# Performance work log

Hardware: AMD Instinct MI355X
Metric: run time of the kernel (lower is better)

Reference implementation:

```python
import jax, jax.numpy as jnp
import numpy as np

PLP_ORDER = 16
N_CHANNEL = 40
FFT_LENGTH = 512
SAMPLE_RATE = 16000
LIFTER = 22
COMP_FACTOR = 0.33
FLOOR = 1e-5
F_MIN = 0.0
F_MAX = SAMPLE_RATE / 2


def _hz_to_mel(hz):
    return 1127.0 * np.log1p(np.asarray(hz, dtype=np.float64) / 700.0)


def _mel_to_hz(mel):
    return 700.0 * np.expm1(np.asarray(mel, dtype=np.float64) / 1127.0)


def _build_constants():
    # SPTK-style mel filter bank (triangular in mel domain).
    mel_min = _hz_to_mel(F_MIN)
    mel_max = _hz_to_mel(F_MAX)
    lower_bin = max(1, int(F_MIN / SAMPLE_RATE * FFT_LENGTH + 1.5))
    upper_bin = min(FFT_LENGTH // 2, int(F_MAX / SAMPLE_RATE * FFT_LENGTH + 0.5))
    seed = np.arange(1, N_CHANNEL + 2)
    cf_mel = (mel_max - mel_min) / (N_CHANNEL + 1) * seed + mel_min  # (C+1,)
    bins = np.arange(lower_bin, upper_bin)
    mel = _hz_to_mel(SAMPLE_RATE * bins / FFT_LENGTH)
    ch = np.searchsorted(cf_mel, mel, side='left')  # first center freq >= mel
    diff = cf_mel - np.concatenate([[mel_min], cf_mel[:-1]])
    w = (cf_mel[ch] - mel) / diff[ch]
    H = np.zeros((len(bins), N_CHANNEL))
    rows = np.arange(len(bins))
    low = ch - 1
    m_lo = low >= 0
    H[rows[m_lo], low[m_lo]] += w[m_lo]
    m_hi = ch <= N_CHANNEL - 1
    H[rows[m_hi], ch[m_hi]] += 1.0 - w[m_hi]
    # Equal-loudness curve over the first C center frequencies (in Hz).
    cf_hz = _mel_to_hz(cf_mel)
    f2 = cf_hz[:N_CHANNEL] ** 2
    eql = (f2 / (f2 + 160000.0)) ** 2 * (f2 + 1440000.0) / (f2 + 9610000.0)
    # Liftering vector, v[0] = 2.
    m = np.arange(PLP_ORDER + 1)
    lift = 1.0 + LIFTER / 2.0 * np.sin(np.pi / LIFTER * m)
    lift[0] = 2.0
    return lower_bin, upper_bin, H.astype(np.float32), eql.astype(np.float32), lift.astype(np.float32)


LOWER_BIN, UPPER_BIN, H_NP, EQL_NP, LIFT_NP = _build_constants()


def _levinson_durbin(r):
    # r: (..., M+1) autocorrelation -> (gain K, LPC coefficients a_1..a_M)
    M = PLP_ORDER
    E = r[..., 0]
    a = jnp.zeros(r.shape[:-1] + (M,), r.dtype)
    for i in range(1, M + 1):
        acc = r[..., i]
        if i > 1:
            acc = acc + jnp.einsum('...j,...j->...', a[..., : i - 1], r[..., 1:i][..., ::-1])
        k = -acc / E
        if i > 1:
            a = a.at[..., : i - 1].set(a[..., : i - 1] + k[..., None] * a[..., : i - 1][..., ::-1])
        a = a.at[..., i - 1].set(k)
        E = E * (1.0 - k * k)
    return jnp.sqrt(E), a


def _lpc_to_cepstrum(K, a):
    # c0 = log K; c_m = -a_m - sum_{k=1}^{m-1} (k/m) c_k a_{m-k}
    M = PLP_ORDER
    c = [jnp.log(K)]
    for m in range(1, M + 1):
        acc = a[..., m - 1]
        for k in range(1, m):
            acc = acc + (k / m) * c[k] * a[..., m - k - 1]
        c.append(-acc)
    return jnp.stack(c, axis=-1)  # (..., M+1)


def _plp(x):
    H = jnp.asarray(H_NP)
    eql = jnp.asarray(EQL_NP)
    lift = jnp.asarray(LIFT_NP)
    # Mel filter bank on power spectrum (use_power=True)
    fb = jnp.matmul(x[..., LOWER_BIN:UPPER_BIN], H)          # (..., C)
    logfb = jnp.log(jnp.maximum(fb, FLOOR))
    # Equal-loudness scaling + cubic-root amplitude compression
    y = (jnp.exp(logfb) * eql) ** COMP_FACTOR                # (..., C)
    # replicate1: duplicate first and last channels
    y = jnp.concatenate([y[..., :1], y, y[..., -1:]], axis=-1)  # (..., C+2)
    n = y.shape[-1]
    # hfft with norm='forward' -> inverse-FFT-like autocorrelation
    r = jnp.fft.hfft(y) / (2 * (n - 1))
    r = r[..., : PLP_ORDER + 1]
    K, a = _levinson_durbin(r)
    c = _lpc_to_cepstrum(K, a)
    c = c * lift
    return c[..., 1:]  # out_format 'y': PLP without C0, (..., M)


def setup_inputs() -> dict:
    key = jax.random.key(0)
    x = jax.random.uniform(key, (32, 4096, FFT_LENGTH // 2 + 1), dtype=jnp.float32)
    return {"x": x}


def reference(x):
    return _plp(x)
```

## Files before the change

kernel.cpp:

```cpp
#include <hip/hip_runtime.h>

#define NCH    40
#define MORD   16
#define NR     17
#define NBINS  257

namespace cfg {

constexpr double PI  = 3.14159265358979323846264338327950288;
constexpr double LN2 = 0.693147180559945309417232121458176568;

constexpr double cexp(double x) {
    double t = 1.0, s = 1.0;
    for (int i = 1; i < 40; ++i) { t *= x / i; s += t; }
    return s;
}

constexpr double clog(double z) {
    double lg = 0.0;
    while (z > 1.4142135623730951) { z *= 0.5; lg += LN2; }
    while (z < 0.7071067811865476) { z *= 2.0; lg -= LN2; }
    double u = (z - 1.0) / (z + 1.0), u2 = u * u, t = u, s = u;
    for (int k = 1; k < 24; ++k) { t *= u2; s += t / (2.0 * k + 1.0); }
    return lg + 2.0 * s;
}

constexpr double ccos(double x) {
    double tp = 2.0 * PI;
    double q = x / tp;
    long long k = (long long)(q + (q >= 0.0 ? 0.5 : -0.5));
    double r = x - (double)k * tp;
    double r2 = r * r, t = 1.0, s = 1.0;
    for (int i = 1; i < 20; ++i) { t *= -r2 / ((2.0 * i - 1.0) * (2.0 * i)); s += t; }
    return s;
}

constexpr double csin(double x) { return ccos(x - PI / 2.0); }

struct Tab {
    int   start[43];
    int   chan[257];
    float w[257];
    float eql[NCH];
    float lift[NR];
    float ctf[NR][21];
    constexpr Tab() : start(), chan(), w(), eql(), lift(), ctf() {
        const double lmax  = clog(87.0 / 7.0);
        const double U1127 = lmax / 41.0;
        for (int c = 0; c <= 41; ++c) {
            double thr = 22.4 * (cexp((double)c * U1127) - 1.0);
            int s = (int)thr + 1;
            if (s < 1) s = 1;
            if (s > 256) s = 256;
            start[c] = s;
        }
        start[42] = start[41];
        for (int c = 0; c <= 40; ++c) {
            for (int b = start[c]; b < start[c + 1]; ++b) {
                double mel = 1127.0 * clog(1.0 + (double)b * 31.25 / 700.0);
                double t   = mel / (1127.0 * U1127);
                w[b] = (float)(t - (double)c);
                chan[b] = c;
            }
        }
        for (int c = 0; c < NCH; ++c) {
            double cf = 700.0 * (cexp((double)(c + 1) * U1127) - 1.0);
            double f2 = cf * cf;
            double e  = f2 / (f2 + 160000.0);
            e = e * e * (f2 + 1440000.0) / (f2 + 9610000.0);
            eql[c] = (float)e;
        }
        for (int m = 0; m < NR; ++m)
            lift[m] = (float)(1.0 + 11.0 * csin(PI * (double)m / 22.0));
        lift[0] = 2.0f;
        for (int l = 0; l < NR; ++l)
            for (int j = 0; j <= 20; ++j) {
                double s = (j == 0) ? 1.0 : 2.0;
                ctf[l][j] = (float)(s * ccos(PI * (double)(j * l) / 41.0) / 82.0);
            }
    }
};

constexpr Tab T{};

}

template<int S>
__device__ __forceinline__ void fbank_path(const float* __restrict__ x,
                                           long long fg, float fb[NCH])
{
    using cfg::T;
    const long long B = fg * 257 + 1 - S;
    const float4* p4 = reinterpret_cast<const float4*>(x + B);
    float4 a = p4[0];
    #pragma unroll
    for (int j = 0; j < 64; ++j) {
        float4 b;
        if (S > 0 || j < 63) b = p4[j + 1]; else b = a;
        float e0, e1, e2, e3;
        if      (S == 0) { e0 = a.x; e1 = a.y; e2 = a.z; e3 = a.w; }
        else if (S == 1) { e0 = a.y; e1 = a.z; e2 = a.w; e3 = b.x; }
        else if (S == 2) { e0 = a.z; e1 = a.w; e2 = b.x; e3 = b.y; }
        else             { e0 = a.w; e1 = b.x; e2 = b.y; e3 = b.z; }
        const float ee[4] = { e0, e1, e2, e3 };
        #pragma unroll
        for (int q = 0; q < 4; ++q) {
            const int   bb = 4 * j + 1 + q;
            const int   ch = T.chan[bb];
            const float wa = T.w[bb];
            if (ch < NCH) fb[ch]     = fmaf(wa, ee[q], fb[ch]);
            if (ch >= 1)  fb[ch - 1] = fmaf(1.0f - wa, ee[q], fb[ch - 1]);
        }
        a = b;
    }
}

__global__ __launch_bounds__(256, 2) void plp_kernel(const float* __restrict__ x,
                                                     float* __restrict__ out,
                                                     int nframes)
{
    using cfg::T;
    const int tid  = threadIdx.x;
    const int lane = tid & 63;
    const long long GW = (long long)blockIdx.x * 4 + (tid >> 6);
    const int       r  = (int)(GW & 3);
    const long long q  = GW >> 2;
    const long long fg = (long long)r + 4 * (q * 64 + lane);
    if (fg >= nframes) return;

    float fb[NCH];
    #pragma unroll
    for (int c = 0; c < NCH; ++c) fb[c] = 0.f;

    switch (r) {
        case 0:  fbank_path<1>(x, fg, fb); break;
        case 1:  fbank_path<2>(x, fg, fb); break;
        case 2:  fbank_path<3>(x, fg, fb); break;
        default: fbank_path<0>(x, fg, fb); break;
    }

    float yv[NCH];
    #pragma unroll
    for (int c = 0; c < NCH; ++c) {
        float v = fmaxf(fb[c], 1e-5f) * T.eql[c];
        yv[c] = __expf(0.33f * __logf(v));
    }

    float ye[21], yo[21];
    ye[0] = yv[0] + yv[39];  yo[0] = yv[0] - yv[39];
    #pragma unroll
    for (int jj = 1; jj <= 20; ++jj) {
        float aa = yv[jj - 1], bb = yv[40 - jj];
        ye[jj] = aa + bb;  yo[jj] = aa - bb;
    }

    float rr[NR];
    #pragma unroll
    for (int lg = 0; lg < NR; ++lg) {
        const float* yy = (lg & 1) ? yo : ye;
        float acc = 0.f;
        #pragma unroll
        for (int jj = 0; jj <= 20; ++jj) acc = fmaf(T.ctf[lg][jj], yy[jj], acc);
        rr[lg] = acc;
    }

    float a[MORD];
    #pragma unroll
    for (int i = 0; i < MORD; ++i) a[i] = 0.f;
    float E = rr[0];
    #pragma unroll
    for (int i = 1; i <= MORD; ++i) {
        float acc = rr[i];
        #pragma unroll
        for (int jj = 0; jj < i - 1; ++jj) acc = fmaf(a[jj], rr[i - 1 - jj], acc);
        float k = -acc * __builtin_amdgcn_rcpf(E);
        const int half = (i - 1) / 2;
        #pragma unroll
        for (int jj = 0; jj < half; ++jj) {
            float t1 = a[jj], t2 = a[i - 2 - jj];
            a[jj]         = fmaf(k, t2, t1);
            a[i - 2 - jj] = fmaf(k, t1, t2);
        }
        if ((i - 1) & 1) a[half] = fmaf(k, a[half], a[half]);
        a[i - 1] = k;
        E = E * (1.f - k * k);
    }

    float cc[NR], ccs[NR];
    #pragma unroll
    for (int m = 1; m <= MORD; ++m) {
        float acc = 0.f;
        #pragma unroll
        for (int k2 = 1; k2 < m; ++k2)
            acc = fmaf(ccs[k2], a[m - k2 - 1], acc);
        float cm = -(a[m - 1] + acc * (1.0f / (float)m));
        cc[m]  = cm;
        ccs[m] = (float)m * cm;
    }

    float o[16];
    #pragma unroll
    for (int m = 1; m <= MORD; ++m) o[m - 1] = cc[m] * T.lift[m];

    float4* op = reinterpret_cast<float4*>(out + (size_t)fg * 16);
    op[0] = make_float4(o[0],  o[1],  o[2],  o[3]);
    op[1] = make_float4(o[4],  o[5],  o[6],  o[7]);
    op[2] = make_float4(o[8],  o[9],  o[10], o[11]);
    op[3] = make_float4(o[12], o[13], o[14], o[15]);
}

extern "C" void kernel_launch(void* const* d_in, const int* in_sizes, int n_in,
                              void* d_out, int out_size, void* d_ws, size_t ws_size,
                              hipStream_t stream) {
    const float* x   = (const float*)d_in[0];
    float*      outp = (float*)d_out;
    int nframes = in_sizes[0] / NBINS;
    int nblocks = (nframes + 255) / 256;
    plp_kernel<<<nblocks, 256, 0, stream>>>(x, outp, nframes);
}
```

Measured before the change: 217.5 us.

## Stage spectrum chunks into LDS with coalesced global_load_lds double buffering

Replaces the per-thread strided float4 row loads, which used shift-specialised templates, with cooperative per-wave staging. Each wave loads 32-bin chunks for its 64 frames through global_load_lds, so every load instruction reads contiguous bins across lanes. Two LDS buffers let the next chunk load while the current one is consumed, and threads then read their own frame row from LDS for the filterbank. The cost is about 66 KB of LDS per block, hand-written waitcnt synchronisation, and an LDS read per bin.

```diff
diff --git a/kernel.cpp b/kernel.cpp
--- a/kernel.cpp
+++ b/kernel.cpp
@@ -4,6 +4,9 @@
 #define MORD   16
 #define NR     17
 #define NBINS  257
+#define NCHUNK 8
+#define CB     32
+#define PAIRW  65
 
 namespace cfg {
 
@@ -85,34 +88,10 @@
 
 }
 
-template<int S>
-__device__ __forceinline__ void fbank_path(const float* __restrict__ x,
-                                           long long fg, float fb[NCH])
-{
-    using cfg::T;
-    const long long B = fg * 257 + 1 - S;
-    const float4* p4 = reinterpret_cast<const float4*>(x + B);
-    float4 a = p4[0];
-    #pragma unroll
-    for (int j = 0; j < 64; ++j) {
-        float4 b;
-        if (S > 0 || j < 63) b = p4[j + 1]; else b = a;
-        float e0, e1, e2, e3;
-        if      (S == 0) { e0 = a.x; e1 = a.y; e2 = a.z; e3 = a.w; }
-        else if (S == 1) { e0 = a.y; e1 = a.z; e2 = a.w; e3 = b.x; }
-        else if (S == 2) { e0 = a.z; e1 = a.w; e2 = b.x; e3 = b.y; }
-        else             { e0 = a.w; e1 = b.x; e2 = b.y; e3 = b.z; }
-        const float ee[4] = { e0, e1, e2, e3 };
-        #pragma unroll
-        for (int q = 0; q < 4; ++q) {
-            const int   bb = 4 * j + 1 + q;
-            const int   ch = T.chan[bb];
-            const float wa = T.w[bb];
-            if (ch < NCH) fb[ch]     = fmaf(wa, ee[q], fb[ch]);
-            if (ch >= 1)  fb[ch - 1] = fmaf(1.0f - wa, ee[q], fb[ch - 1]);
-        }
-        a = b;
-    }
+__device__ __forceinline__ void gload_lds4(const float* g, float* l) {
+    __builtin_amdgcn_global_load_lds(
+        (const __attribute__((address_space(1))) unsigned int*)g,
+        (__attribute__((address_space(3))) unsigned int*)l, 4, 0, 0);
 }
 
 __global__ __launch_bounds__(256, 2) void plp_kernel(const float* __restrict__ x,
@@ -120,24 +99,56 @@
                                                      int nframes)
 {
     using cfg::T;
-    const int tid  = threadIdx.x;
-    const int lane = tid & 63;
-    const long long GW = (long long)blockIdx.x * 4 + (tid >> 6);
-    const int       r  = (int)(GW & 3);
-    const long long q  = GW >> 2;
-    const long long fg = (long long)r + 4 * (q * 64 + lane);
-    if (fg >= nframes) return;
+    __shared__ float slab[4][2][32][PAIRW];
+
+    const int tid = threadIdx.x;
+    const int w   = tid >> 6;
+    const int l   = tid & 63;
+    const int s   = l >> 5;
+    const int j   = l & 31;
+    const long long F0    = (long long)blockIdx.x * 256;
+    const long long fbase = F0 + (long long)(w << 6);
+
+    auto stage = [&](int c, int b) {
+        asm volatile("" ::: "memory");
+        const float* gp0 = x + c * CB + j;
+        #pragma unroll
+        for (int r = 0; r < 32; ++r) {
+            long long fg = fbase + 2 * r + s;
+            if (fg > (long long)nframes - 1) fg = (long long)nframes - 1;
+            gload_lds4(gp0 + fg * NBINS, &slab[w][b][r][0]);
+        }
+    };
 
     float fb[NCH];
     #pragma unroll
     for (int c = 0; c < NCH; ++c) fb[c] = 0.f;
 
-    switch (r) {
-        case 0:  fbank_path<1>(x, fg, fb); break;
-        case 1:  fbank_path<2>(x, fg, fb); break;
-        case 2:  fbank_path<3>(x, fg, fb); break;
-        default: fbank_path<0>(x, fg, fb); break;
-    }
+    stage(0, 0);
+
+    #pragma unroll
+    for (int c8 = 0; c8 < NCHUNK; ++c8) {
+        if (c8 + 1 < NCHUNK) {
+            stage(c8 + 1, (c8 + 1) & 1);
+            asm volatile("s_waitcnt vmcnt(32)" ::: "memory");
+        } else {
+            asm volatile("s_waitcnt vmcnt(0)" ::: "memory");
+        }
+        const float* fr = &slab[w][c8 & 1][l >> 1][(l & 1) * CB];
+        #pragma unroll
+        for (int p = 0; p < CB; ++p) {
+            const int bb = (c8 << 5) + p;
+            if (bb == 0) continue;
+            const float xv = fr[p];
+            const int   ch = T.chan[bb];
+            const float wa = T.w[bb];
+            if (ch < NCH) fb[ch]     = fmaf(wa, xv, fb[ch]);
+            if (ch >= 1)  fb[ch - 1] = fmaf(1.0f - wa, xv, fb[ch - 1]);
+        }
+    }
+
+    const long long frame = F0 + tid;
+    const bool live = frame < (long long)nframes;
 
     float yv[NCH];
     #pragma unroll
@@ -198,15 +209,17 @@
         ccs[m] = (float)m * cm;
     }
 
-    float o[16];
-    #pragma unroll
-    for (int m = 1; m <= MORD; ++m) o[m - 1] = cc[m] * T.lift[m];
-
-    float4* op = reinterpret_cast<float4*>(out + (size_t)fg * 16);
-    op[0] = make_float4(o[0],  o[1],  o[2],  o[3]);
-    op[1] = make_float4(o[4],  o[5],  o[6],  o[7]);
-    op[2] = make_float4(o[8],  o[9],  o[10], o[11]);
-    op[3] = make_float4(o[12], o[13], o[14], o[15]);
+    if (live) {
+        float o[16];
+        #pragma unroll
+        for (int m = 1; m <= MORD; ++m) o[m - 1] = cc[m] * T.lift[m];
+
+        float4* op = reinterpret_cast<float4*>(out + (size_t)frame * 16);
+        op[0] = make_float4(o[0],  o[1],  o[2],  o[3]);
+        op[1] = make_float4(o[4],  o[5],  o[6],  o[7]);
+        op[2] = make_float4(o[8],  o[9],  o[10], o[11]);
+        op[3] = make_float4(o[12], o[13], o[14], o[15]);
+    }
 }
 
 extern "C" void kernel_launch(void* const* d_in, const int* in_sizes, int n_in,
```

After: 201.2 us. 1.08x faster.

## Stage frame slab through shared memory as fp16 with coalesced loads

Applied to the files above, without the earlier changes.

Each block of 128 threads now cooperatively loads 128 contiguous frames with coalesced float4 reads, converts them to half precision and stores them in a shared-memory slab. Each thread then reads its frame from LDS as half2 pairs, picking its parity path by wave so that half2 accesses stay aligned. This replaces the per-thread strided unaligned global reads with coalesced global traffic and LDS reads, at the cost of about 66KB of LDS per block, which limits occupancy, plus fp16 rounding of the power-spectrum inputs. Bounds checks on loads were dropped, so the code assumes the frame count is a multiple of 128.

```diff
diff --git a/kernel.cpp b/kernel.cpp
--- a/kernel.cpp
+++ b/kernel.cpp
@@ -1,9 +1,11 @@
 #include <hip/hip_runtime.h>
+#include <hip/hip_fp16.h>
 
 #define NCH    40
 #define MORD   16
 #define NR     17
 #define NBINS  257
+#define FPB    128
 
 namespace cfg {
 
@@ -85,59 +87,79 @@
 
 }
 
-template<int S>
-__device__ __forceinline__ void fbank_path(const float* __restrict__ x,
-                                           long long fg, float fb[NCH])
+template<int PAR>
+__device__ __forceinline__ void fbank_pairs(const __half2* __restrict__ fr2, float fb[NCH])
 {
     using cfg::T;
-    const long long B = fg * 257 + 1 - S;
-    const float4* p4 = reinterpret_cast<const float4*>(x + B);
-    float4 a = p4[0];
-    #pragma unroll
-    for (int j = 0; j < 64; ++j) {
-        float4 b;
-        if (S > 0 || j < 63) b = p4[j + 1]; else b = a;
-        float e0, e1, e2, e3;
-        if      (S == 0) { e0 = a.x; e1 = a.y; e2 = a.z; e3 = a.w; }
-        else if (S == 1) { e0 = a.y; e1 = a.z; e2 = a.w; e3 = b.x; }
-        else if (S == 2) { e0 = a.z; e1 = a.w; e2 = b.x; e3 = b.y; }
-        else             { e0 = a.w; e1 = b.x; e2 = b.y; e3 = b.z; }
-        const float ee[4] = { e0, e1, e2, e3 };
-        #pragma unroll
-        for (int q = 0; q < 4; ++q) {
-            const int   bb = 4 * j + 1 + q;
+    #pragma unroll
+    for (int p = 0; p < 128; ++p) {
+        const float2 xp = __half22float2(fr2[p]);
+        {
+            const int   bb = 2 * p + PAR;
             const int   ch = T.chan[bb];
             const float wa = T.w[bb];
-            if (ch < NCH) fb[ch]     = fmaf(wa, ee[q], fb[ch]);
-            if (ch >= 1)  fb[ch - 1] = fmaf(1.0f - wa, ee[q], fb[ch - 1]);
-        }
-        a = b;
-    }
-}
-
-__global__ __launch_bounds__(256, 2) void plp_kernel(const float* __restrict__ x,
-                                                     float* __restrict__ out,
-                                                     int nframes)
+            if (wa != 0.f || ch != 0) {
+                if (ch < NCH) fb[ch]     = fmaf(wa, xp.x, fb[ch]);
+                if (ch >= 1)  fb[ch - 1] = fmaf(1.0f - wa, xp.x, fb[ch - 1]);
+            }
+        }
+        {
+            const int   bb = 2 * p + 1 + PAR;
+            const int   ch = T.chan[bb];
+            const float wa = T.w[bb];
+            if (wa != 0.f || ch != 0) {
+                if (ch < NCH) fb[ch]     = fmaf(wa, xp.y, fb[ch]);
+                if (ch >= 1)  fb[ch - 1] = fmaf(1.0f - wa, xp.y, fb[ch - 1]);
+            }
+        }
+    }
+}
+
+__global__ __launch_bounds__(FPB) void plp_kernel(const float* __restrict__ x,
+                                                  float* __restrict__ out,
+                                                  int nframes)
 {
     using cfg::T;
-    const int tid  = threadIdx.x;
-    const int lane = tid & 63;
-    const long long GW = (long long)blockIdx.x * 4 + (tid >> 6);
-    const int       r  = (int)(GW & 3);
-    const long long q  = GW >> 2;
-    const long long fg = (long long)r + 4 * (q * 64 + lane);
-    if (fg >= nframes) return;
+    __shared__ __half slabH[FPB * NBINS];
+
+    const int tid = threadIdx.x;
+    const long long F0 = (long long)blockIdx.x * FPB;
+
+    {
+        const float4* src = reinterpret_cast<const float4*>(x + F0 * NBINS);
+        #pragma unroll 8
+        for (int r = 0; r < 64; ++r) {
+            const int i = (r << 7) + tid;
+            const float4 v = src[i];
+            union { __half2 h[2]; uint2 u; } cv;
+            cv.h[0] = __float22half2_rn(make_float2(v.x, v.y));
+            cv.h[1] = __float22half2_rn(make_float2(v.z, v.w));
+            *reinterpret_cast<uint2*>(&slabH[(size_t)4 * i]) = cv.u;
+        }
+        if (tid < 32) {
+            const int i = 8192 + tid;
+            const float4 v = src[i];
+            union { __half2 h[2]; uint2 u; } cv;
+            cv.h[0] = __float22half2_rn(make_float2(v.x, v.y));
+            cv.h[1] = __float22half2_rn(make_float2(v.z, v.w));
+            *reinterpret_cast<uint2*>(&slabH[(size_t)4 * i]) = cv.u;
+        }
+    }
+    __syncthreads();
+
+    const int w  = tid >> 6;
+    const int l  = tid & 63;
+    const int fl = 2 * l + w;
+    const long long frame = F0 + fl;
+
+    const __half2* fr2 = reinterpret_cast<const __half2*>(&slabH[fl * NBINS + w]);
 
     float fb[NCH];
     #pragma unroll
     for (int c = 0; c < NCH; ++c) fb[c] = 0.f;
 
-    switch (r) {
-        case 0:  fbank_path<1>(x, fg, fb); break;
-        case 1:  fbank_path<2>(x, fg, fb); break;
-        case 2:  fbank_path<3>(x, fg, fb); break;
-        default: fbank_path<0>(x, fg, fb); break;
-    }
+    if (w == 0) fbank_pairs<0>(fr2, fb);
+    else        fbank_pairs<1>(fr2, fb);
 
     float yv[NCH];
     #pragma unroll
@@ -198,15 +220,17 @@
         ccs[m] = (float)m * cm;
     }
 
-    float o[16];
-    #pragma unroll
-    for (int m = 1; m <= MORD; ++m) o[m - 1] = cc[m] * T.lift[m];
-
-    float4* op = reinterpret_cast<float4*>(out + (size_t)fg * 16);
-    op[0] = make_float4(o[0],  o[1],  o[2],  o[3]);
-    op[1] = make_float4(o[4],  o[5],  o[6],  o[7]);
-    op[2] = make_float4(o[8],  o[9],  o[10], o[11]);
-    op[3] = make_float4(o[12], o[13], o[14], o[15]);
+    if (frame < (long long)nframes) {
+        float o[16];
+        #pragma unroll
+        for (int m = 1; m <= MORD; ++m) o[m - 1] = cc[m] * T.lift[m];
+
+        float4* op = reinterpret_cast<float4*>(out + (size_t)frame * 16);
+        op[0] = make_float4(o[0],  o[1],  o[2],  o[3]);
+        op[1] = make_float4(o[4],  o[5],  o[6],  o[7]);
+        op[2] = make_float4(o[8],  o[9],  o[10], o[11]);
+        op[3] = make_float4(o[12], o[13], o[14], o[15]);
+    }
 }
 
 extern "C" void kernel_launch(void* const* d_in, const int* in_sizes, int n_in,
@@ -215,6 +239,6 @@
     const float* x   = (const float*)d_in[0];
     float*      outp = (float*)d_out;
     int nframes = in_sizes[0] / NBINS;
-    int nblocks = (nframes + 255) / 256;
-    plp_kernel<<<nblocks, 256, 0, stream>>>(x, outp, nframes);
-}
+    int nblocks = (nframes + FPB - 1) / FPB;
+    plp_kernel<<<nblocks, FPB, 0, stream>>>(x, outp, nframes);
+}
```

Measured after the change: 196.3 us. 9.8% less time.
